# Kernel optimization log

Measured on AMD Instinct MI355X. Metric: run time of the kernel, lower is better.

The kernel has to match this reference:

```python
import jax, jax.numpy as jnp
import numpy as np

B, S, D, H = 2, 2048, 2048, 16
HD = D // H  # head_dim = 128


def setup_inputs() -> dict:
    key = jax.random.key(0)
    ks = jax.random.split(key, 9)
    std = 0.02
    x = jax.random.normal(ks[0], (B, S, D), dtype=jnp.float32)
    Wq = jax.random.normal(ks[1], (D, D), dtype=jnp.float32) * std
    bq = jnp.zeros((D,), dtype=jnp.float32)
    Wk = jax.random.normal(ks[2], (D, D), dtype=jnp.float32) * std
    bk = jnp.zeros((D,), dtype=jnp.float32)
    Wv = jax.random.normal(ks[3], (D, D), dtype=jnp.float32) * std
    bv = jnp.zeros((D,), dtype=jnp.float32)
    Wo = jax.random.normal(ks[4], (D, D), dtype=jnp.float32) * std
    bo = jnp.zeros((D,), dtype=jnp.float32)
    return {"x": x, "Wq": Wq, "bq": bq, "Wk": Wk, "bk": bk,
            "Wv": Wv, "bv": bv, "Wo": Wo, "bo": bo}


def _rope_tables(seq_len, head_dim, base=10000.0):
    # inv_freq over even indices; freqs: [S, HD/2]
    inv_freq = 1.0 / (base ** (jnp.arange(0, head_dim, 2, dtype=jnp.float32) / head_dim))
    t = jnp.arange(seq_len, dtype=jnp.float32)
    freqs = jnp.einsum('i,j->ij', t, inv_freq)
    return jnp.cos(freqs), jnp.sin(freqs)  # each [S, HD/2]


def _rotate(x, cos, sin):
    # x: [B, H, S, HD]; cos/sin: [S, HD/2] broadcast over B,H
    x1, x2 = jnp.split(x, 2, axis=-1)
    return jnp.concatenate([x1 * cos - x2 * sin, x1 * sin + x2 * cos], axis=-1)


def reference(x, Wq, bq, Wk, bk, Wv, bv, Wo, bo):
    b, s, d = x.shape
    q = (jnp.einsum('bsd,df->bsf', x, Wq) + bq).reshape(b, s, H, HD).transpose(0, 2, 1, 3)
    k = (jnp.einsum('bsd,df->bsf', x, Wk) + bk).reshape(b, s, H, HD).transpose(0, 2, 1, 3)
    v = (jnp.einsum('bsd,df->bsf', x, Wv) + bv).reshape(b, s, H, HD).transpose(0, 2, 1, 3)
    cos, sin = _rope_tables(s, HD)
    qr = _rotate(q, cos, sin)
    kr = _rotate(k, cos, sin)
    scores = jnp.einsum('bhqd,bhkd->bhqk', qr, kr) / jnp.sqrt(jnp.float32(HD))
    probs = jax.nn.softmax(scores, axis=-1)
    out = jnp.einsum('bhqk,bhkd->bhqd', probs, v)
    out = out.transpose(0, 2, 1, 3).reshape(b, s, d)
    return jnp.einsum('bsd,df->bsf', out, Wo) + bo
```

## Files before the change

kernel.cpp:

```cpp
#include <hip/hip_runtime.h>

#define BB  2
#define SS  2048
#define DD  2048
#define HH  16
#define HDD 128
#define BSR 4096

using short8  = __attribute__((ext_vector_type(8))) short;
using floatx4 = __attribute__((ext_vector_type(4))) float;

__device__ __forceinline__ float bf2f(unsigned short u) {
  return __uint_as_float(((unsigned int)u) << 16);
}
__device__ __forceinline__ unsigned short f2bf(float f) {
  unsigned int u = __float_as_uint(f);
  u += 0x7fffu + ((u >> 16) & 1u);
  return (unsigned short)(u >> 16);
}
__device__ __forceinline__ unsigned int pk2bf(float a, float b) {
  unsigned int ua = __float_as_uint(a);
  ua += 0x7fffu + ((ua >> 16) & 1u);
  unsigned int ub = __float_as_uint(b);
  ub += 0x7fffu + ((ub >> 16) & 1u);
  return (ua >> 16) | (ub & 0xffff0000u);
}
__device__ __forceinline__ void gl_lds16(const void* g, void* l) {
  __builtin_amdgcn_global_load_lds(
      (__attribute__((address_space(1))) void*)g,
      (__attribute__((address_space(3))) void*)l, 16, 0, 0);
}

__global__ __launch_bounds__(256) void transpose_w(
    const float* __restrict__ Wq, const float* __restrict__ Wk,
    const float* __restrict__ Wv, const float* __restrict__ Wo,
    unsigned short* __restrict__ wqkvt, unsigned short* __restrict__ wot)
{
  __shared__ float tile[32][33];
  const float* W; unsigned short* Out;
  int z = blockIdx.z;
  if      (z == 0) { W = Wq; Out = wqkvt; }
  else if (z == 1) { W = Wk; Out = wqkvt + (size_t)DD * DD; }
  else if (z == 2) { W = Wv; Out = wqkvt + 2 * (size_t)DD * DD; }
  else             { W = Wo; Out = wot; }
  int tx = threadIdx.x, ty = threadIdx.y;
  int d0 = blockIdx.y * 32, f0 = blockIdx.x * 32;
#pragma unroll
  for (int i = 0; i < 4; i++)
    tile[ty + i * 8][tx] = W[(size_t)(d0 + ty + i * 8) * DD + f0 + tx];
  __syncthreads();
#pragma unroll
  for (int i = 0; i < 4; i++)
    Out[(size_t)(f0 + ty + i * 8) * DD + d0 + tx] = f2bf(tile[tx][ty + i * 8]);
}

__global__ __launch_bounds__(256) void conv_x(const float* __restrict__ x,
                                              unsigned short* __restrict__ xb)
{
  size_t i = ((size_t)blockIdx.x * 256 + threadIdx.x) * 4;
  float4 v = *(const float4*)(x + i);
  ushort4 o;
  o.x = f2bf(v.x); o.y = f2bf(v.y); o.z = f2bf(v.z); o.w = f2bf(v.w);
  *(ushort4*)(xb + i) = o;
}

template <bool OUTF32>
__global__ __launch_bounds__(256) void gemm_bt(
    const unsigned short* __restrict__ A, const unsigned short* __restrict__ Bt,
    const float* __restrict__ bias, void* __restrict__ Cout,
    int M, int N, int K)
{
  __shared__ unsigned short As[128 * 32];
  __shared__ unsigned short Bs[128 * 32];
  int t = threadIdx.x;
  int m0 = blockIdx.y * 128, n0 = blockIdx.x * 128;
  int w = t >> 6, lane = t & 63, qd = lane >> 4, l16 = lane & 15;
  int wm = (w >> 1) * 64, wn = (w & 1) * 64;
  floatx4 zero4 = {0.f, 0.f, 0.f, 0.f};
  floatx4 acc[4][4];
#pragma unroll
  for (int i = 0; i < 4; i++)
#pragma unroll
    for (int j = 0; j < 4; j++) acc[i][j] = zero4;

  int gchunk = (t & 3) ^ ((t >> 3) & 3);
  const unsigned short* Ab = A  + (size_t)(m0 + (t >> 2)) * K + gchunk * 8;
  const unsigned short* Bb = Bt + (size_t)(n0 + (t >> 2)) * K + gchunk * 8;
  size_t half = (size_t)64 * K;
  int cswz = (qd ^ ((l16 >> 1) & 3)) * 8;

  for (int k0 = 0; k0 < K; k0 += 32) {
    __syncthreads();
    gl_lds16(Ab + k0,        &As[t * 8]);
    gl_lds16(Ab + half + k0, &As[2048 + t * 8]);
    gl_lds16(Bb + k0,        &Bs[t * 8]);
    gl_lds16(Bb + half + k0, &Bs[2048 + t * 8]);
    __syncthreads();
    short8 af[4], bfr[4];
#pragma unroll
    for (int i = 0; i < 4; i++)
      af[i] = *(const short8*)&As[(wm + i * 16 + l16) * 32 + cswz];
#pragma unroll
    for (int j = 0; j < 4; j++)
      bfr[j] = *(const short8*)&Bs[(wn + j * 16 + l16) * 32 + cswz];
#pragma unroll
    for (int i = 0; i < 4; i++)
#pragma unroll
      for (int j = 0; j < 4; j++)
        acc[i][j] = __builtin_amdgcn_mfma_f32_16x16x32_bf16(af[i], bfr[j], acc[i][j], 0, 0, 0);
  }

#pragma unroll
  for (int i = 0; i < 4; i++)
#pragma unroll
    for (int j = 0; j < 4; j++) {
      int row = m0 + wm + i * 16 + qd * 4;
      int col = n0 + wn + j * 16 + l16;
      float bsv = bias ? bias[col] : 0.f;
#pragma unroll
      for (int r = 0; r < 4; r++) {
        float v = acc[i][j][r] + bsv;
        if (OUTF32) ((float*)Cout)[(size_t)(row + r) * N + col] = v;
        else ((unsigned short*)Cout)[(size_t)(row + r) * N + col] = f2bf(v);
      }
    }
}

__global__ __launch_bounds__(256) void rope_qk(
    const unsigned short* __restrict__ qkv, const float* __restrict__ bq,
    const float* __restrict__ bk, unsigned short* __restrict__ q_r,
    unsigned short* __restrict__ k_r)
{
  int lin = blockIdx.x * 256 + threadIdx.x;
  int i = lin & 63;
  int s = (lin >> 6) & (SS - 1);
  int h = (lin >> 17) & (HH - 1);
  int b = lin >> 21;
  size_t row = (size_t)(b * SS + s) * (3 * DD);
  int f = h * HDD + i;
  float q1 = bf2f(qkv[row + f])            + bq[f];
  float q2 = bf2f(qkv[row + f + 64])       + bq[f + 64];
  float k1 = bf2f(qkv[row + DD + f])       + bk[f];
  float k2 = bf2f(qkv[row + DD + f + 64])  + bk[f + 64];
  float inv = powf(10000.f, -(float)i * (1.f / 64.f));
  float ang = (float)s * inv;
  float sn, c;
  sincosf(ang, &sn, &c);
  const float qs = 0.08838834764831845f;
  size_t ob = ((size_t)(b * HH + h) * SS + s) * HDD;
  q_r[ob + i]      = f2bf((q1 * c - q2 * sn) * qs);
  q_r[ob + i + 64] = f2bf((q1 * sn + q2 * c) * qs);
  k_r[ob + i]      = f2bf(k1 * c - k2 * sn);
  k_r[ob + i + 64] = f2bf(k1 * sn + k2 * c);
}

__global__ __launch_bounds__(256) void v_transpose(
    const unsigned short* __restrict__ qkv, const float* __restrict__ bv,
    unsigned short* __restrict__ v_t)
{
  __shared__ float tile[32][33];
  int bh = blockIdx.z; int b = bh >> 4, h = bh & 15;
  int s0 = blockIdx.x * 32, d0 = blockIdx.y * 32;
  int tx = threadIdx.x, ty = threadIdx.y;
#pragma unroll
  for (int i = 0; i < 4; i++) {
    int s = s0 + ty + i * 8, dh = d0 + tx;
    tile[ty + i * 8][tx] =
        bf2f(qkv[(size_t)(b * SS + s) * (3 * DD) + 2 * DD + h * HDD + dh]) + bv[h * HDD + dh];
  }
  __syncthreads();
  int s = s0 + tx;
  int y = s & 63;
  int kap = ((y >> 5) & 1) * 32 + ((y >> 2) & 3) * 8 + ((y >> 4) & 1) * 4 + (y & 3);
  int scol = (s & ~63) + kap;
#pragma unroll
  for (int i = 0; i < 4; i++)
    v_t[((size_t)(b * HH + h) * HDD + d0 + ty + i * 8) * SS + scol] =
        f2bf(tile[tx][ty + i * 8]);
}

__global__ __launch_bounds__(256, 2) void attn_kernel(
    const unsigned short* __restrict__ q_r, const unsigned short* __restrict__ k_r,
    const unsigned short* __restrict__ v_t, unsigned short* __restrict__ aout)
{
  __shared__ unsigned short Ks[64 * 128];
  __shared__ unsigned short Vs[128 * 64];
  int t = threadIdx.x, w = t >> 6, lane = t & 63, qd = lane >> 4, l16 = lane & 15;
  int bh = blockIdx.y, q0 = blockIdx.x * 128;
  const unsigned short* qb = q_r + (size_t)bh * SS * HDD;
  const unsigned short* kb = k_r + (size_t)bh * SS * HDD;
  const unsigned short* vb = v_t + (size_t)bh * HDD * SS;

  short8 aq[2][4];
#pragma unroll
  for (int mi = 0; mi < 2; mi++)
#pragma unroll
    for (int ks = 0; ks < 4; ks++)
      aq[mi][ks] = *(const short8*)
          &qb[(size_t)(q0 + w * 32 + mi * 16 + l16) * HDD + ks * 32 + qd * 8];

  float m_i[2], l_i[2];
  floatx4 zero4 = {0.f, 0.f, 0.f, 0.f};
  floatx4 o[2][8];
#pragma unroll
  for (int mi = 0; mi < 2; mi++) { m_i[mi] = -1e30f; l_i[mi] = 0.f; }
#pragma unroll
  for (int mi = 0; mi < 2; mi++)
#pragma unroll
    for (int n = 0; n < 8; n++) o[mi][n] = zero4;

  for (int kt = 0; kt < SS; kt += 64) {
    __syncthreads();
#pragma unroll
    for (int c = 0; c < 4; c++) {
      int flat = c * 256 + t;
      int r = flat >> 4, cc = flat & 15;
      gl_lds16(kb + (size_t)(kt + r) * HDD + (cc ^ (r & 15)) * 8, &Ks[flat * 8]);
    }
#pragma unroll
    for (int c = 0; c < 4; c++) {
      int flat = c * 256 + t;
      int r = flat >> 3, cc = flat & 7;
      gl_lds16(vb + (size_t)r * SS + kt + (cc ^ (r & 7)) * 8, &Vs[flat * 8]);
    }
    __syncthreads();

    floatx4 sc[2][4];
#pragma unroll
    for (int mi = 0; mi < 2; mi++)
#pragma unroll
      for (int j = 0; j < 4; j++) sc[mi][j] = zero4;
#pragma unroll
    for (int j = 0; j < 4; j++) {
      int krow = j * 16 + l16;
#pragma unroll
      for (int ks = 0; ks < 4; ks++) {
        int chunk = ks * 4 + qd;
        short8 kf = *(const short8*)&Ks[krow * 128 + ((chunk ^ (krow & 15)) * 8)];
        sc[0][j] = __builtin_amdgcn_mfma_f32_16x16x32_bf16(kf, aq[0][ks], sc[0][j], 0, 0, 0);
        sc[1][j] = __builtin_amdgcn_mfma_f32_16x16x32_bf16(kf, aq[1][ks], sc[1][j], 0, 0, 0);
      }
    }

    float rmax[2];
#pragma unroll
    for (int mi = 0; mi < 2; mi++) {
      float m = sc[mi][0][0];
#pragma unroll
      for (int j = 0; j < 4; j++)
#pragma unroll
        for (int r = 0; r < 4; r++) m = fmaxf(m, sc[mi][j][r]);
      m = fmaxf(m, __shfl_xor(m, 16, 64));
      m = fmaxf(m, __shfl_xor(m, 32, 64));
      rmax[mi] = m;
    }

    bool up = (rmax[0] > m_i[0]) || (rmax[1] > m_i[1]);
    if (__ballot(up) != 0ull) {
#pragma unroll
      for (int mi = 0; mi < 2; mi++) {
        float mn = fmaxf(m_i[mi], rmax[mi]);
        float a = __expf(m_i[mi] - mn);
        m_i[mi] = mn;
        l_i[mi] *= a;
#pragma unroll
        for (int n = 0; n < 8; n++)
#pragma unroll
          for (int r = 0; r < 4; r++) o[mi][n][r] *= a;
      }
    }

    unsigned int pr[2][4][2];
#pragma unroll
    for (int mi = 0; mi < 2; mi++) {
      float s0 = 0.f;
#pragma unroll
      for (int j = 0; j < 4; j++) {
        float p0 = __expf(sc[mi][j][0] - m_i[mi]);
        float p1 = __expf(sc[mi][j][1] - m_i[mi]);
        float p2 = __expf(sc[mi][j][2] - m_i[mi]);
        float p3 = __expf(sc[mi][j][3] - m_i[mi]);
        s0 += (p0 + p1) + (p2 + p3);
        pr[mi][j][0] = pk2bf(p0, p1);
        pr[mi][j][1] = pk2bf(p2, p3);
      }
      s0 += __shfl_xor(s0, 16, 64);
      s0 += __shfl_xor(s0, 32, 64);
      l_i[mi] += s0;
    }

#pragma unroll
    for (int n = 0; n < 8; n++) {
      int vrow = n * 16 + l16;
#pragma unroll
      for (int ks = 0; ks < 2; ks++) {
        int chunk = ks * 4 + qd;
        short8 av = *(const short8*)&Vs[vrow * 64 + ((chunk ^ (vrow & 7)) * 8)];
        union { unsigned int u[4]; short8 v; } bp0, bp1;
        bp0.u[0] = pr[0][2 * ks][0];     bp0.u[1] = pr[0][2 * ks][1];
        bp0.u[2] = pr[0][2 * ks + 1][0]; bp0.u[3] = pr[0][2 * ks + 1][1];
        bp1.u[0] = pr[1][2 * ks][0];     bp1.u[1] = pr[1][2 * ks][1];
        bp1.u[2] = pr[1][2 * ks + 1][0]; bp1.u[3] = pr[1][2 * ks + 1][1];
        o[0][n] = __builtin_amdgcn_mfma_f32_16x16x32_bf16(av, bp0.v, o[0][n], 0, 0, 0);
        o[1][n] = __builtin_amdgcn_mfma_f32_16x16x32_bf16(av, bp1.v, o[1][n], 0, 0, 0);
      }
    }
  }

  int b = bh >> 4, h = bh & 15;
#pragma unroll
  for (int mi = 0; mi < 2; mi++) {
    int qrow = q0 + w * 32 + mi * 16 + l16;
    float inv_l = 1.f / l_i[mi];
    size_t base = ((size_t)(b * SS + qrow)) * DD + h * HDD;
#pragma unroll
    for (int n = 0; n < 8; n++) {
      uint2 pkd;
      pkd.x = pk2bf(o[mi][n][0] * inv_l, o[mi][n][1] * inv_l);
      pkd.y = pk2bf(o[mi][n][2] * inv_l, o[mi][n][3] * inv_l);
      *(uint2*)&aout[base + n * 16 + qd * 4] = pkd;
    }
  }
}

extern "C" void kernel_launch(void* const* d_in, const int* in_sizes, int n_in,
                              void* d_out, int out_size, void* d_ws, size_t ws_size,
                              hipStream_t stream) {
  const float* x  = (const float*)d_in[0];
  const float* Wq = (const float*)d_in[1];
  const float* bq = (const float*)d_in[2];
  const float* Wk = (const float*)d_in[3];
  const float* bk = (const float*)d_in[4];
  const float* Wv = (const float*)d_in[5];
  const float* bv = (const float*)d_in[6];
  const float* Wo = (const float*)d_in[7];
  const float* bo = (const float*)d_in[8];
  float* out = (float*)d_out;

  char* ws = (char*)d_ws;
  unsigned short* xb      = (unsigned short*)(ws + 0);
  unsigned short* wqkvt   = (unsigned short*)(ws + 16777216);
  unsigned short* wot     = (unsigned short*)(ws + 41943040);
  unsigned short* qkv     = (unsigned short*)(ws + 50331648);
  unsigned short* q_r     = (unsigned short*)(ws + 100663296);
  unsigned short* k_r     = (unsigned short*)(ws + 117440512);
  unsigned short* v_t     = (unsigned short*)(ws + 134217728);
  unsigned short* attn_o  = xb;

  transpose_w<<<dim3(DD / 32, DD / 32, 4), dim3(32, 8), 0, stream>>>(
      Wq, Wk, Wv, Wo, wqkvt, wot);
  conv_x<<<dim3((BSR * DD) / 1024), dim3(256), 0, stream>>>(x, xb);
  gemm_bt<false><<<dim3(3 * DD / 128, BSR / 128), dim3(256), 0, stream>>>(
      xb, wqkvt, nullptr, qkv, BSR, 3 * DD, DD);
  rope_qk<<<dim3((BB * HH * SS * 64) / 256), dim3(256), 0, stream>>>(
      qkv, bq, bk, q_r, k_r);
  v_transpose<<<dim3(SS / 32, HDD / 32, BB * HH), dim3(32, 8), 0, stream>>>(
      qkv, bv, v_t);
  attn_kernel<<<dim3(SS / 128, BB * HH), dim3(256), 0, stream>>>(
      q_r, k_r, v_t, attn_o);
  gemm_bt<true><<<dim3(DD / 128, BSR / 128), dim3(256), 0, stream>>>(
      attn_o, wot, bo, out, BSR, DD, DD);
}
```

Baseline: 459.3 us.

## Double-buffer attention K/V tiles, remap blocks per XCD, widen GEMM K-tile

The attention kernel now keeps two LDS buffers for K and V. The next 64-key tile is issued into the idle buffer while the current one is consumed, so there is one barrier per iteration instead of two. Blocks are remapped so that all query tiles of a head share `L&7`, which on round-robin XCD dispatch should keep each head's K/V in one L2. The GEMM K-step grows from 32 to 64 with an 8-way XOR swizzle, halving the barrier count per output tile. The cost is doubled LDS use in both kernels (64KB per attention block), which may limit occupancy.

New measurement: 443.7 us. -3.4%, faster.

```diff
diff --git a/kernel.cpp b/kernel.cpp
--- a/kernel.cpp
+++ b/kernel.cpp
@@ -70,8 +70,8 @@
     const float* __restrict__ bias, void* __restrict__ Cout,
     int M, int N, int K)
 {
-  __shared__ unsigned short As[128 * 32];
-  __shared__ unsigned short Bs[128 * 32];
+  __shared__ unsigned short As[128 * 64];
+  __shared__ unsigned short Bs[128 * 64];
   int t = threadIdx.x;
   int m0 = blockIdx.y * 128, n0 = blockIdx.x * 128;
   int w = t >> 6, lane = t & 63, qd = lane >> 4, l16 = lane & 15;
@@ -83,31 +83,35 @@
 #pragma unroll
     for (int j = 0; j < 4; j++) acc[i][j] = zero4;
 
-  int gchunk = (t & 3) ^ ((t >> 3) & 3);
-  const unsigned short* Ab = A  + (size_t)(m0 + (t >> 2)) * K + gchunk * 8;
-  const unsigned short* Bb = Bt + (size_t)(n0 + (t >> 2)) * K + gchunk * 8;
-  size_t half = (size_t)64 * K;
-  int cswz = (qd ^ ((l16 >> 1) & 3)) * 8;
-
-  for (int k0 = 0; k0 < K; k0 += 32) {
+  int gchunk = (t & 7) ^ ((t >> 3) & 7);
+  const unsigned short* Ab = A  + (size_t)(m0 + (t >> 3)) * K + gchunk * 8;
+  const unsigned short* Bb = Bt + (size_t)(n0 + (t >> 3)) * K + gchunk * 8;
+  size_t qK = (size_t)32 * K;
+
+  for (int k0 = 0; k0 < K; k0 += 64) {
     __syncthreads();
-    gl_lds16(Ab + k0,        &As[t * 8]);
-    gl_lds16(Ab + half + k0, &As[2048 + t * 8]);
-    gl_lds16(Bb + k0,        &Bs[t * 8]);
-    gl_lds16(Bb + half + k0, &Bs[2048 + t * 8]);
+#pragma unroll
+    for (int c = 0; c < 4; c++) {
+      gl_lds16(Ab + c * qK + k0, &As[(c * 256 + t) * 8]);
+      gl_lds16(Bb + c * qK + k0, &Bs[(c * 256 + t) * 8]);
+    }
     __syncthreads();
-    short8 af[4], bfr[4];
-#pragma unroll
-    for (int i = 0; i < 4; i++)
-      af[i] = *(const short8*)&As[(wm + i * 16 + l16) * 32 + cswz];
-#pragma unroll
-    for (int j = 0; j < 4; j++)
-      bfr[j] = *(const short8*)&Bs[(wn + j * 16 + l16) * 32 + cswz];
-#pragma unroll
-    for (int i = 0; i < 4; i++)
+#pragma unroll
+    for (int ks = 0; ks < 2; ks++) {
+      int ch = ((ks * 4 + qd) ^ (l16 & 7)) * 8;
+      short8 af[4], bfr[4];
+#pragma unroll
+      for (int i = 0; i < 4; i++)
+        af[i] = *(const short8*)&As[(wm + i * 16 + l16) * 64 + ch];
 #pragma unroll
       for (int j = 0; j < 4; j++)
-        acc[i][j] = __builtin_amdgcn_mfma_f32_16x16x32_bf16(af[i], bfr[j], acc[i][j], 0, 0, 0);
+        bfr[j] = *(const short8*)&Bs[(wn + j * 16 + l16) * 64 + ch];
+#pragma unroll
+      for (int i = 0; i < 4; i++)
+#pragma unroll
+        for (int j = 0; j < 4; j++)
+          acc[i][j] = __builtin_amdgcn_mfma_f32_16x16x32_bf16(af[i], bfr[j], acc[i][j], 0, 0, 0);
+    }
   }
 
 #pragma unroll
@@ -183,10 +187,13 @@
     const unsigned short* __restrict__ q_r, const unsigned short* __restrict__ k_r,
     const unsigned short* __restrict__ v_t, unsigned short* __restrict__ aout)
 {
-  __shared__ unsigned short Ks[64 * 128];
-  __shared__ unsigned short Vs[128 * 64];
+  __shared__ unsigned short Ks[2][64 * 128];
+  __shared__ unsigned short Vs[2][128 * 64];
   int t = threadIdx.x, w = t >> 6, lane = t & 63, qd = lane >> 4, l16 = lane & 15;
-  int bh = blockIdx.y, q0 = blockIdx.x * 128;
+  int L = blockIdx.y * gridDim.x + blockIdx.x;
+  int jj = L >> 3;
+  int bh = (L & 7) * 4 + (jj >> 4);
+  int q0 = (jj & 15) * 128;
   const unsigned short* qb = q_r + (size_t)bh * SS * HDD;
   const unsigned short* kb = k_r + (size_t)bh * SS * HDD;
   const unsigned short* vb = v_t + (size_t)bh * HDD * SS;
@@ -209,21 +216,27 @@
 #pragma unroll
     for (int n = 0; n < 8; n++) o[mi][n] = zero4;
 
-  for (int kt = 0; kt < SS; kt += 64) {
-    __syncthreads();
+  auto stage = [&](int nb, int kt) {
 #pragma unroll
     for (int c = 0; c < 4; c++) {
       int flat = c * 256 + t;
       int r = flat >> 4, cc = flat & 15;
-      gl_lds16(kb + (size_t)(kt + r) * HDD + (cc ^ (r & 15)) * 8, &Ks[flat * 8]);
+      gl_lds16(kb + (size_t)(kt + r) * HDD + (cc ^ (r & 15)) * 8, &Ks[nb][flat * 8]);
     }
 #pragma unroll
     for (int c = 0; c < 4; c++) {
       int flat = c * 256 + t;
       int r = flat >> 3, cc = flat & 7;
-      gl_lds16(vb + (size_t)r * SS + kt + (cc ^ (r & 7)) * 8, &Vs[flat * 8]);
-    }
+      gl_lds16(vb + (size_t)r * SS + kt + (cc ^ (r & 7)) * 8, &Vs[nb][flat * 8]);
+    }
+  };
+
+  stage(0, 0);
+  int buf = 0;
+
+  for (int kt = 0; kt < SS; kt += 64) {
     __syncthreads();
+    if (kt + 64 < SS) stage(buf ^ 1, kt + 64);
 
     floatx4 sc[2][4];
 #pragma unroll
@@ -236,7 +249,7 @@
 #pragma unroll
       for (int ks = 0; ks < 4; ks++) {
         int chunk = ks * 4 + qd;
-        short8 kf = *(const short8*)&Ks[krow * 128 + ((chunk ^ (krow & 15)) * 8)];
+        short8 kf = *(const short8*)&Ks[buf][krow * 128 + ((chunk ^ (krow & 15)) * 8)];
         sc[0][j] = __builtin_amdgcn_mfma_f32_16x16x32_bf16(kf, aq[0][ks], sc[0][j], 0, 0, 0);
         sc[1][j] = __builtin_amdgcn_mfma_f32_16x16x32_bf16(kf, aq[1][ks], sc[1][j], 0, 0, 0);
       }
@@ -295,7 +308,7 @@
 #pragma unroll
       for (int ks = 0; ks < 2; ks++) {
         int chunk = ks * 4 + qd;
-        short8 av = *(const short8*)&Vs[vrow * 64 + ((chunk ^ (vrow & 7)) * 8)];
+        short8 av = *(const short8*)&Vs[buf][vrow * 64 + ((chunk ^ (vrow & 7)) * 8)];
         union { unsigned int u[4]; short8 v; } bp0, bp1;
         bp0.u[0] = pr[0][2 * ks][0];     bp0.u[1] = pr[0][2 * ks][1];
         bp0.u[2] = pr[0][2 * ks + 1][0]; bp0.u[3] = pr[0][2 * ks + 1][1];
@@ -305,6 +318,7 @@
         o[1][n] = __builtin_amdgcn_mfma_f32_16x16x32_bf16(av, bp1.v, o[1][n], 0, 0, 0);
       }
     }
+    buf ^= 1;
   }
 
   int b = bh >> 4, h = bh & 15;
```
